# Optimization experiments

Measured on AMD Instinct MI355X. Metric: run time of the kernel, lower is better.

## Reference

```python
import jax, jax.numpy as jnp
import numpy as np

# Faithful JAX port of the approxmatch algorithm (Fan et al. / PyTorch-EMDLoss CUDA kernel):
# iterative soft bipartite matching with annealed temperature levels -4^j for j=8..-1, then 0,
# tracking remaining capacities ('saturation') of both point sets.

EPS = 1e-9

def _approx_match(xyz1, xyz2):
    # xyz1: [B,N,D], xyz2: [B,M,D] -> match: [B,N,M]
    B, n, _ = xyz1.shape
    m = xyz2.shape[1]
    factorl = max(n, m) // n  # capacity per point in set 1
    factorr = max(n, m) // m  # capacity per point in set 2
    # pairwise squared distances [B,N,M]
    d2 = jnp.sum((xyz1[:, :, None, :] - xyz2[:, None, :, :]) ** 2, axis=-1)
    # annealing levels: -4^8, -4^7, ..., -4^-1, 0
    levels = jnp.array([-(4.0 ** j) for j in range(8, -2, -1)] + [0.0],
                       dtype=xyz1.dtype)
    satl0 = jnp.full((B, n), float(factorl), dtype=xyz1.dtype)
    satr0 = jnp.full((B, m), float(factorr), dtype=xyz1.dtype)
    match0 = jnp.zeros((B, n, m), dtype=xyz1.dtype)

    def step(carry, level):
        satl, satr, match = carry
        # soft assignment weights scaled by remaining capacity of set 2
        w = jnp.exp(level * d2) * satr[:, None, :]                      # [B,N,M]
        # row-normalize, scaled by remaining capacity of set 1
        w = w / (jnp.sum(w, axis=2, keepdims=True) + EPS) * satl[:, :, None]
        # column capacity clipping
        ss = jnp.sum(w, axis=1) + EPS                                   # [B,M]
        r = jnp.minimum(satr / ss, 1.0)
        w = w * r[:, None, :]
        satr = jnp.maximum(satr - jnp.sum(w, axis=1), 0.0)
        satl = jnp.maximum(satl - jnp.sum(w, axis=2), 0.0)
        return (satl, satr, match + w), None

    (_, _, match), _ = jax.lax.scan(step, (satl0, satr0, match0), levels)
    return match


def setup_inputs() -> dict:
    key = jax.random.key(0)
    k1, k2 = jax.random.split(key)
    xyz1 = jax.random.normal(k1, (8, 2048, 3), dtype=jnp.float32)
    xyz2 = jax.random.normal(k2, (8, 2048, 3), dtype=jnp.float32)
    return {"xyz1": xyz1, "xyz2": xyz2}


def reference(xyz1, xyz2):
    # EMD cost per batch element: sum_{k,l} match[k,l] * ||x1_k - x2_l||
    match = _approx_match(xyz1, xyz2)                                   # [B,N,M]
    d = jnp.sqrt(jnp.sum((xyz1[:, :, None, :] - xyz2[:, None, :, :]) ** 2,
                         axis=-1))                                      # [B,N,M]
    return jnp.sum(match * d, axis=(1, 2))                              # [B]
```

## Files before the change

### kernel.cpp

```cpp
#include <hip/hip_runtime.h>
#include <math.h>

static constexpr int   B_   = 8;
static constexpr int   N_   = 2048;
static constexpr int   TPB  = 256;
static constexpr int   TILE = 32;
static constexpr int   NBLK = (B_ * N_) / TILE;
static constexpr int   BN   = B_ * N_;
static constexpr float EPS_ = 1e-9f;

#define WS_X1    (ws)
#define WS_X2    (ws + 4*BN)
#define WS_SATL  (ws + 8*BN)
#define WS_SATR  (ws + 9*BN)
#define WS_SCAL  (ws + 10*BN)
#define WS_LSCAL (ws + 11*BN)
#define WS_LSATR (ws + 12*BN)
#define WS_WR    (ws + 13*BN)
#define WS_LWR   (ws + 14*BN)
#define WS_COST  (ws + 15*BN)

__global__ void __launch_bounds__(TPB)
emd_init(const float* __restrict__ xyz1, const float* __restrict__ xyz2,
         float* __restrict__ ws)
{
    const int idx = blockIdx.x * TPB + threadIdx.x;
    if (idx >= BN) return;
    float x = xyz1[idx*3], y = xyz1[idx*3+1], z = xyz1[idx*3+2];
    reinterpret_cast<float4*>(WS_X1)[idx] =
        make_float4(x, y, z, fmaf(x,x, fmaf(y,y, z*z)));
    x = xyz2[idx*3]; y = xyz2[idx*3+1]; z = xyz2[idx*3+2];
    reinterpret_cast<float4*>(WS_X2)[idx] =
        make_float4(x, y, z, fmaf(x,x, fmaf(y,y, z*z)));
    WS_SATL[idx] = 1.f;
    WS_SATR[idx] = 1.f;
    WS_LSATR[idx] = 0.f;
    WS_COST[idx] = 0.f;
}

template<int MODE>
__global__ void __launch_bounds__(TPB)
emd_pass(float* __restrict__ ws, const float lvlA, const float lvlB)
{
    __shared__ float4 pts[N_];
    __shared__ float  auxA[N_];
    __shared__ float  auxB[N_];
    __shared__ float  red[64][33];

    const int b    = blockIdx.x >> 6;
    const int tile = blockIdx.x & 63;
    const int t    = threadIdx.x;
    const int g    = t & 3;
    const int c    = t >> 2;

    const float4* src = (MODE == 1)
        ? reinterpret_cast<const float4*>(WS_X1) + b * N_
        : reinterpret_cast<const float4*>(WS_X2) + b * N_;
    const float* aA = (MODE == 0) ? (WS_LSATR + b * N_)
                     : (MODE == 1) ? (WS_LSCAL + b * N_)
                     : (MODE == 2) ? (WS_LWR   + b * N_)
                                   : (WS_WR    + b * N_);
    const float* aB = WS_LSATR + b * N_;
    for (int p = t; p < N_; p += TPB) {
        pts[p]  = src[p];
        auxA[p] = aA[p];
        if (MODE == 2) auxB[p] = aB[p];
    }

    const float4* ownv = (MODE == 1)
        ? reinterpret_cast<const float4*>(WS_X2)
        : reinterpret_cast<const float4*>(WS_X1);
    const int obase = b * N_ + tile * TILE + g * 8;
    float cx[8], cy[8], cz[8], cq[8];
#pragma unroll
    for (int j = 0; j < 8; ++j) {
        float4 v = ownv[obase + j];
        cx[j] = -2.f * v.x; cy[j] = -2.f * v.y; cz[j] = -2.f * v.z;
        cq[j] = v.w;
    }
    __syncthreads();

    float s1[8], s2[8], s3[8];
#pragma unroll
    for (int j = 0; j < 8; ++j) { s1[j] = 0.f; s2[j] = 0.f; s3[j] = 0.f; }

    for (int i = 0; i < 32; ++i) {
        const int l = c + (i << 6);
        const float4 p = pts[l];
        const float  wA = auxA[l];
        float wB;
        if (MODE == 2) wB = auxB[l];
#pragma unroll
        for (int j = 0; j < 8; ++j) {
            const float s0 = p.w + cq[j];
            const float d2 = fmaf(cx[j], p.x,
                             fmaf(cy[j], p.y,
                             fmaf(cz[j], p.z, s0)));
            if (MODE == 0 || MODE == 1) {
                s1[j] += __builtin_amdgcn_exp2f(fmaf(lvlB, d2, wA));
            } else if (MODE == 2) {
                const float sq = __builtin_amdgcn_sqrtf(fmaxf(d2, 0.f));
                const float eA = __builtin_amdgcn_exp2f(fmaf(lvlA, d2, wA));
                s1[j] += eA;
                s2[j]  = fmaf(eA, sq, s2[j]);
                s3[j] += __builtin_amdgcn_exp2f(fmaf(lvlB, d2, wB));
            } else {
                const float sq = __builtin_amdgcn_sqrtf(fmaxf(d2, 0.f));
                s2[j] = fmaf(wA, sq, s2[j]);
            }
        }
    }

    float rs1 = 0.f, rs2 = 0.f, rs3 = 0.f;
    if (MODE != 3) {
#pragma unroll
        for (int j = 0; j < 8; ++j) red[c][g * 8 + j] = s1[j];
        __syncthreads();
        if (t < TILE) for (int cc = 0; cc < 64; ++cc) rs1 += red[cc][t];
    }
    if (MODE >= 2) {
        if (MODE != 3) __syncthreads();
#pragma unroll
        for (int j = 0; j < 8; ++j) red[c][g * 8 + j] = s2[j];
        __syncthreads();
        if (t < TILE) for (int cc = 0; cc < 64; ++cc) rs2 += red[cc][t];
    }
    if (MODE == 2) {
        __syncthreads();
#pragma unroll
        for (int j = 0; j < 8; ++j) red[c][g * 8 + j] = s3[j];
        __syncthreads();
        if (t < TILE) for (int cc = 0; cc < 64; ++cc) rs3 += red[cc][t];
    }

    if (t < TILE) {
        const int idx = b * N_ + tile * TILE + t;
        if (MODE == 0) {
            const float sc = WS_SATL[idx] / (rs1 + EPS_);
            WS_SCAL[idx]  = sc;
            WS_LSCAL[idx] = __log2f(sc);
        } else if (MODE == 1) {
            const float sr  = WS_SATR[idx];
            const float w1s = sr * rs1;
            const float rr  = fminf(sr / (w1s + EPS_), 1.f);
            const float wrv = sr * rr;
            const float srn = fmaxf(sr - rr * w1s, 0.f);
            WS_WR[idx]    = wrv;
            WS_LWR[idx]   = __log2f(wrv);
            WS_SATR[idx]  = srn;
            WS_LSATR[idx] = __log2f(srn);
        } else if (MODE == 2) {
            const float scp  = WS_SCAL[idx];
            const float sln  = fmaxf(WS_SATL[idx] - scp * rs1, 0.f);
            WS_COST[idx]     = fmaf(scp, rs2, WS_COST[idx]);
            const float scn  = sln / (rs3 + EPS_);
            WS_SATL[idx]  = sln;
            WS_SCAL[idx]  = scn;
            WS_LSCAL[idx] = __log2f(scn);
        } else {
            WS_COST[idx] = fmaf(WS_SCAL[idx], rs2, WS_COST[idx]);
        }
    }
}

__global__ void __launch_bounds__(TPB)
emd_finish(const float* __restrict__ cost, float* __restrict__ out)
{
    const int b = blockIdx.x;
    const int t = threadIdx.x;
    float v = 0.f;
    for (int i = t; i < N_; i += TPB) v += cost[b * N_ + i];
#pragma unroll
    for (int k = 32; k >= 1; k >>= 1) v += __shfl_xor(v, k, 64);
    __shared__ float wsum[4];
    if ((t & 63) == 0) wsum[t >> 6] = v;
    __syncthreads();
    if (t == 0) out[b] = wsum[0] + wsum[1] + wsum[2] + wsum[3];
}

extern "C" void kernel_launch(void* const* d_in, const int* in_sizes, int n_in,
                              void* d_out, int out_size, void* d_ws, size_t ws_size,
                              hipStream_t stream)
{
    const float* xyz1 = (const float*)d_in[0];
    const float* xyz2 = (const float*)d_in[1];
    float* out = (float*)d_out;
    float* ws  = (float*)d_ws;

    emd_init<<<BN / TPB, TPB, 0, stream>>>(xyz1, xyz2, ws);

    static const float levels[11] = {
        -65536.f, -16384.f, -4096.f, -1024.f, -256.f,
        -64.f, -16.f, -4.f, -1.f, -0.25f, 0.f};
    const float LOG2E = 1.4426950408889634f;

    emd_pass<0><<<NBLK, TPB, 0, stream>>>(ws, 0.f, levels[0] * LOG2E);
    emd_pass<1><<<NBLK, TPB, 0, stream>>>(ws, 0.f, levels[0] * LOG2E);
    for (int lev = 1; lev < 11; ++lev) {
        emd_pass<2><<<NBLK, TPB, 0, stream>>>(ws, levels[lev-1] * LOG2E,
                                                  levels[lev]   * LOG2E);
        emd_pass<1><<<NBLK, TPB, 0, stream>>>(ws, 0.f, levels[lev] * LOG2E);
    }
    emd_pass<3><<<NBLK, TPB, 0, stream>>>(ws, 0.f, 0.f);

    emd_finish<<<B_, TPB, 0, stream>>>(WS_COST, out);
}
```

Measured before the change: 352.3 us.

## Fuse all annealing passes into one persistent kernel with per-batch grid barriers

Replaces the 23 separate pass launches and the finish kernel with a single persistent kernel. Its 512 blocks sync per batch through atomic counter barriers, and per-point saturation, scale and cost stay in registers instead of round-tripping through global memory. The level factor is folded into the precomputed coefficients and shared-memory aux arrays, which saves a multiply per pair, and the block reduction becomes two-stage. The risks are deadlock if not all blocks are co-resident (it relies on 2 blocks per CU, with a spin timeout), plus barrier spin overhead.

```diff
diff --git a/kernel.cpp b/kernel.cpp
--- a/kernel.cpp
+++ b/kernel.cpp
@@ -5,47 +5,112 @@
 static constexpr int   N_   = 2048;
 static constexpr int   TPB  = 256;
 static constexpr int   TILE = 32;
-static constexpr int   NBLK = (B_ * N_) / TILE;
+static constexpr int   BPB  = 64;
+static constexpr int   NBLK = B_ * BPB;
 static constexpr int   BN   = B_ * N_;
 static constexpr float EPS_ = 1e-9f;
+static constexpr float LOG2E = 1.4426950408889634f;
 
 #define WS_X1    (ws)
 #define WS_X2    (ws + 4*BN)
-#define WS_SATL  (ws + 8*BN)
-#define WS_SATR  (ws + 9*BN)
-#define WS_SCAL  (ws + 10*BN)
-#define WS_LSCAL (ws + 11*BN)
-#define WS_LSATR (ws + 12*BN)
-#define WS_WR    (ws + 13*BN)
-#define WS_LWR   (ws + 14*BN)
-#define WS_COST  (ws + 15*BN)
+#define WS_LSCAL (ws + 8*BN)
+#define WS_LSATR (ws + 9*BN)
+#define WS_LWR   (ws + 10*BN)
+#define WS_WR    (ws + 11*BN)
+#define WS_COSTP (ws + 12*BN)
+#define WS_BARU  ((unsigned*)(ws + 12*BN + NBLK))
+
+__device__ __constant__ float c_lvl[11] = {
+    -65536.f*LOG2E, -16384.f*LOG2E, -4096.f*LOG2E, -1024.f*LOG2E,
+    -256.f*LOG2E,   -64.f*LOG2E,    -16.f*LOG2E,   -4.f*LOG2E,
+    -1.f*LOG2E,     -0.25f*LOG2E,   0.f };
 
 __global__ void __launch_bounds__(TPB)
 emd_init(const float* __restrict__ xyz1, const float* __restrict__ xyz2,
          float* __restrict__ ws)
 {
     const int idx = blockIdx.x * TPB + threadIdx.x;
-    if (idx >= BN) return;
-    float x = xyz1[idx*3], y = xyz1[idx*3+1], z = xyz1[idx*3+2];
-    reinterpret_cast<float4*>(WS_X1)[idx] =
-        make_float4(x, y, z, fmaf(x,x, fmaf(y,y, z*z)));
-    x = xyz2[idx*3]; y = xyz2[idx*3+1]; z = xyz2[idx*3+2];
-    reinterpret_cast<float4*>(WS_X2)[idx] =
-        make_float4(x, y, z, fmaf(x,x, fmaf(y,y, z*z)));
-    WS_SATL[idx] = 1.f;
-    WS_SATR[idx] = 1.f;
-    WS_LSATR[idx] = 0.f;
-    WS_COST[idx] = 0.f;
+    if (idx < BN) {
+        float x = xyz1[idx*3], y = xyz1[idx*3+1], z = xyz1[idx*3+2];
+        reinterpret_cast<float4*>(WS_X1)[idx] =
+            make_float4(x, y, z, fmaf(x,x, fmaf(y,y, z*z)));
+        x = xyz2[idx*3]; y = xyz2[idx*3+1]; z = xyz2[idx*3+2];
+        reinterpret_cast<float4*>(WS_X2)[idx] =
+            make_float4(x, y, z, fmaf(x,x, fmaf(y,y, z*z)));
+        WS_LSATR[idx] = 0.f;
+    }
+    if (idx < 8 * 64) WS_BARU[idx] = 0u;
+}
+
+__device__ __forceinline__ void bbar(unsigned* cnt, unsigned* gen, unsigned target)
+{
+    __syncthreads();
+    if (threadIdx.x == 0) {
+        __threadfence();
+        unsigned prev = __hip_atomic_fetch_add(cnt, 1u, __ATOMIC_ACQ_REL,
+                                               __HIP_MEMORY_SCOPE_AGENT);
+        if (prev == BPB - 1) {
+            __hip_atomic_store(cnt, 0u, __ATOMIC_RELAXED, __HIP_MEMORY_SCOPE_AGENT);
+            __hip_atomic_fetch_add(gen, 1u, __ATOMIC_ACQ_REL, __HIP_MEMORY_SCOPE_AGENT);
+        } else {
+            int spins = 0;
+            while (__hip_atomic_load(gen, __ATOMIC_ACQUIRE,
+                                     __HIP_MEMORY_SCOPE_AGENT) < target) {
+                __builtin_amdgcn_s_sleep(1);
+                if (++spins > (1 << 26)) break;
+            }
+        }
+        __threadfence();
+    }
+    __syncthreads();
 }
 
 template<int MODE>
-__global__ void __launch_bounds__(TPB)
-emd_pass(float* __restrict__ ws, const float lvlA, const float lvlB)
+__device__ __forceinline__ void sweep(
+    const float4* pts, const float* auxA, const float* auxB,
+    const float (&kx)[8], const float (&ky)[8], const float (&kz)[8],
+    const float (&kq)[8], float lvlA, float lvlB, int c,
+    float (&s1)[8], float (&s2)[8], float (&s3)[8])
+{
+    for (int i = 0; i < 32; ++i) {
+        const int l = c + (i << 6);
+        const float4 p = pts[l];
+        const float  wA = auxA[l];
+        float wB = 0.f;
+        if (MODE == 2) wB = auxB[l];
+#pragma unroll
+        for (int j = 0; j < 8; ++j) {
+            if (MODE == 0 || MODE == 1) {
+                const float arg = fmaf(kx[j], p.x, fmaf(ky[j], p.y,
+                                  fmaf(kz[j], p.z, wA + kq[j])));
+                s1[j] += __builtin_amdgcn_exp2f(arg);
+            } else if (MODE == 2) {
+                const float dotq = fmaf(kx[j], p.x, fmaf(ky[j], p.y,
+                                   fmaf(kz[j], p.z, kq[j])));
+                const float sq = __builtin_amdgcn_sqrtf(fmaxf(p.w + dotq, 0.f));
+                const float eA = __builtin_amdgcn_exp2f(fmaf(lvlA, dotq, wA));
+                const float eB = __builtin_amdgcn_exp2f(fmaf(lvlB, dotq, wB));
+                s1[j] += eA;
+                s2[j]  = fmaf(eA, sq, s2[j]);
+                s3[j] += eB;
+            } else {
+                const float dotq = fmaf(kx[j], p.x, fmaf(ky[j], p.y,
+                                   fmaf(kz[j], p.z, kq[j])));
+                const float sq = __builtin_amdgcn_sqrtf(fmaxf(p.w + dotq, 0.f));
+                s2[j] = fmaf(wA, sq, s2[j]);
+            }
+        }
+    }
+}
+
+__global__ void __launch_bounds__(TPB, 2)
+emd_main(float* __restrict__ ws, float* __restrict__ out)
 {
     __shared__ float4 pts[N_];
     __shared__ float  auxA[N_];
     __shared__ float  auxB[N_];
     __shared__ float  red[64][33];
+    __shared__ float  red2[8][33];
 
     const int b    = blockIdx.x >> 6;
     const int tile = blockIdx.x & 63;
@@ -53,129 +118,143 @@
     const int g    = t & 3;
     const int c    = t >> 2;
 
-    const float4* src = (MODE == 1)
-        ? reinterpret_cast<const float4*>(WS_X1) + b * N_
-        : reinterpret_cast<const float4*>(WS_X2) + b * N_;
-    const float* aA = (MODE == 0) ? (WS_LSATR + b * N_)
-                     : (MODE == 1) ? (WS_LSCAL + b * N_)
-                     : (MODE == 2) ? (WS_LWR   + b * N_)
-                                   : (WS_WR    + b * N_);
-    const float* aB = WS_LSATR + b * N_;
-    for (int p = t; p < N_; p += TPB) {
-        pts[p]  = src[p];
-        auxA[p] = aA[p];
-        if (MODE == 2) auxB[p] = aB[p];
-    }
-
-    const float4* ownv = (MODE == 1)
-        ? reinterpret_cast<const float4*>(WS_X2)
-        : reinterpret_cast<const float4*>(WS_X1);
-    const int obase = b * N_ + tile * TILE + g * 8;
-    float cx[8], cy[8], cz[8], cq[8];
-#pragma unroll
-    for (int j = 0; j < 8; ++j) {
-        float4 v = ownv[obase + j];
-        cx[j] = -2.f * v.x; cy[j] = -2.f * v.y; cz[j] = -2.f * v.z;
-        cq[j] = v.w;
-    }
-    __syncthreads();
-
+    unsigned* bcnt = WS_BARU + b * 64;
+    unsigned* bgen = bcnt + 32;
+    unsigned  mygen = 0;
+
+    const float4* x1v = reinterpret_cast<const float4*>(WS_X1) + b * N_;
+    const float4* x2v = reinterpret_cast<const float4*>(WS_X2) + b * N_;
+    const float* lscal = WS_LSCAL + b * N_;
+    const float* lsatr = WS_LSATR + b * N_;
+    const float* lwr   = WS_LWR   + b * N_;
+    const float* wrr   = WS_WR    + b * N_;
+
+    float rx[8], ry[8], rz[8], rq[8], ox[8], oy[8], oz[8], oq[8];
+    {
+        const int ob = tile * TILE + g * 8;
+#pragma unroll
+        for (int j = 0; j < 8; ++j) {
+            float4 v = x1v[ob + j];
+            rx[j] = -2.f*v.x; ry[j] = -2.f*v.y; rz[j] = -2.f*v.z; rq[j] = v.w;
+            float4 w = x2v[ob + j];
+            ox[j] = -2.f*w.x; oy[j] = -2.f*w.y; oz[j] = -2.f*w.z; oq[j] = w.w;
+        }
+    }
+
+    float satl = 1.f, satr = 1.f, mysc = 0.f, cost = 0.f;
+    const int gidx = b * N_ + tile * TILE + t;
     float s1[8], s2[8], s3[8];
-#pragma unroll
+    float kx[8], ky[8], kz[8], kq[8];
+
+#define ZERO3() _Pragma("unroll") \
     for (int j = 0; j < 8; ++j) { s1[j] = 0.f; s2[j] = 0.f; s3[j] = 0.f; }
 
-    for (int i = 0; i < 32; ++i) {
-        const int l = c + (i << 6);
-        const float4 p = pts[l];
-        const float  wA = auxA[l];
-        float wB;
-        if (MODE == 2) wB = auxB[l];
+#define REDUCE(arr, dst)                                                   \
+    {   _Pragma("unroll")                                                  \
+        for (int j = 0; j < 8; ++j) red[c][g * 8 + j] = arr[j];            \
+        __syncthreads();                                                   \
+        { const int o = t & 31, sg = t >> 5; float a = 0.f;                \
+          _Pragma("unroll")                                                \
+          for (int k = 0; k < 8; ++k) a += red[sg * 8 + k][o];             \
+          red2[sg][o] = a; }                                               \
+        __syncthreads();                                                   \
+        dst = 0.f;                                                         \
+        if (t < TILE) { _Pragma("unroll")                                  \
+            for (int sgg = 0; sgg < 8; ++sgg) dst += red2[sgg][t]; }       \
+        __syncthreads(); }
+
+    {
+        const float lv = c_lvl[0];
+        for (int p = t; p < N_; p += TPB) {
+            float4 v = x2v[p]; pts[p] = v;
+            auxA[p] = fmaf(lv, v.w, lsatr[p]);
+        }
 #pragma unroll
         for (int j = 0; j < 8; ++j) {
-            const float s0 = p.w + cq[j];
-            const float d2 = fmaf(cx[j], p.x,
-                             fmaf(cy[j], p.y,
-                             fmaf(cz[j], p.z, s0)));
-            if (MODE == 0 || MODE == 1) {
-                s1[j] += __builtin_amdgcn_exp2f(fmaf(lvlB, d2, wA));
-            } else if (MODE == 2) {
-                const float sq = __builtin_amdgcn_sqrtf(fmaxf(d2, 0.f));
-                const float eA = __builtin_amdgcn_exp2f(fmaf(lvlA, d2, wA));
-                s1[j] += eA;
-                s2[j]  = fmaf(eA, sq, s2[j]);
-                s3[j] += __builtin_amdgcn_exp2f(fmaf(lvlB, d2, wB));
-            } else {
-                const float sq = __builtin_amdgcn_sqrtf(fmaxf(d2, 0.f));
-                s2[j] = fmaf(wA, sq, s2[j]);
-            }
-        }
-    }
-
-    float rs1 = 0.f, rs2 = 0.f, rs3 = 0.f;
-    if (MODE != 3) {
-#pragma unroll
-        for (int j = 0; j < 8; ++j) red[c][g * 8 + j] = s1[j];
+            kx[j] = lv*rx[j]; ky[j] = lv*ry[j]; kz[j] = lv*rz[j]; kq[j] = lv*rq[j];
+        }
         __syncthreads();
-        if (t < TILE) for (int cc = 0; cc < 64; ++cc) rs1 += red[cc][t];
-    }
-    if (MODE >= 2) {
-        if (MODE != 3) __syncthreads();
-#pragma unroll
-        for (int j = 0; j < 8; ++j) red[c][g * 8 + j] = s2[j];
-        __syncthreads();
-        if (t < TILE) for (int cc = 0; cc < 64; ++cc) rs2 += red[cc][t];
-    }
-    if (MODE == 2) {
-        __syncthreads();
-#pragma unroll
-        for (int j = 0; j < 8; ++j) red[c][g * 8 + j] = s3[j];
-        __syncthreads();
-        if (t < TILE) for (int cc = 0; cc < 64; ++cc) rs3 += red[cc][t];
-    }
-
-    if (t < TILE) {
-        const int idx = b * N_ + tile * TILE + t;
-        if (MODE == 0) {
-            const float sc = WS_SATL[idx] / (rs1 + EPS_);
-            WS_SCAL[idx]  = sc;
-            WS_LSCAL[idx] = __log2f(sc);
-        } else if (MODE == 1) {
-            const float sr  = WS_SATR[idx];
-            const float w1s = sr * rs1;
-            const float rr  = fminf(sr / (w1s + EPS_), 1.f);
-            const float wrv = sr * rr;
-            const float srn = fmaxf(sr - rr * w1s, 0.f);
-            WS_WR[idx]    = wrv;
-            WS_LWR[idx]   = __log2f(wrv);
-            WS_SATR[idx]  = srn;
-            WS_LSATR[idx] = __log2f(srn);
-        } else if (MODE == 2) {
-            const float scp  = WS_SCAL[idx];
-            const float sln  = fmaxf(WS_SATL[idx] - scp * rs1, 0.f);
-            WS_COST[idx]     = fmaf(scp, rs2, WS_COST[idx]);
-            const float scn  = sln / (rs3 + EPS_);
-            WS_SATL[idx]  = sln;
-            WS_SCAL[idx]  = scn;
-            WS_LSCAL[idx] = __log2f(scn);
+        ZERO3();
+        sweep<0>(pts, auxA, auxB, kx, ky, kz, kq, 0.f, 0.f, c, s1, s2, s3);
+        float rs1; REDUCE(s1, rs1);
+        if (t < TILE) {
+            mysc = satl / (rs1 + EPS_);
+            WS_LSCAL[gidx] = __log2f(mysc);
+        }
+        bbar(bcnt, bgen, ++mygen);
+    }
+
+    for (int lev = 0; lev <= 10; ++lev) {
+        {
+            const float lv = c_lvl[lev];
+            for (int p = t; p < N_; p += TPB) {
+                float4 v = x1v[p]; pts[p] = v;
+                auxA[p] = fmaf(lv, v.w, lscal[p]);
+            }
+#pragma unroll
+            for (int j = 0; j < 8; ++j) {
+                kx[j] = lv*ox[j]; ky[j] = lv*oy[j]; kz[j] = lv*oz[j]; kq[j] = lv*oq[j];
+            }
+            __syncthreads();
+            ZERO3();
+            sweep<1>(pts, auxA, auxB, kx, ky, kz, kq, 0.f, 0.f, c, s1, s2, s3);
+            float rs1; REDUCE(s1, rs1);
+            if (t < TILE) {
+                const float w1s = satr * rs1;
+                const float rr  = fminf(satr / (w1s + EPS_), 1.f);
+                const float wrv = satr * rr;
+                satr = fmaxf(satr - rr * w1s, 0.f);
+                WS_WR[gidx]    = wrv;
+                WS_LWR[gidx]   = __log2f(wrv);
+                WS_LSATR[gidx] = __log2f(satr);
+            }
+            bbar(bcnt, bgen, ++mygen);
+        }
+
+        if (lev < 10) {
+            const float lvA = c_lvl[lev], lvB = c_lvl[lev + 1];
+            for (int p = t; p < N_; p += TPB) {
+                float4 v = x2v[p]; pts[p] = v;
+                auxA[p] = fmaf(lvA, v.w, lwr[p]);
+                auxB[p] = fmaf(lvB, v.w, lsatr[p]);
+            }
+            __syncthreads();
+            ZERO3();
+            sweep<2>(pts, auxA, auxB, rx, ry, rz, rq, lvA, lvB, c, s1, s2, s3);
+            float rs1, rs2, rs3;
+            REDUCE(s1, rs1); REDUCE(s2, rs2); REDUCE(s3, rs3);
+            if (t < TILE) {
+                satl = fmaxf(satl - mysc * rs1, 0.f);
+                cost = fmaf(mysc, rs2, cost);
+                mysc = satl / (rs3 + EPS_);
+                WS_LSCAL[gidx] = __log2f(mysc);
+            }
+            bbar(bcnt, bgen, ++mygen);
         } else {
-            WS_COST[idx] = fmaf(WS_SCAL[idx], rs2, WS_COST[idx]);
-        }
-    }
-}
-
-__global__ void __launch_bounds__(TPB)
-emd_finish(const float* __restrict__ cost, float* __restrict__ out)
-{
-    const int b = blockIdx.x;
-    const int t = threadIdx.x;
-    float v = 0.f;
-    for (int i = t; i < N_; i += TPB) v += cost[b * N_ + i];
-#pragma unroll
-    for (int k = 32; k >= 1; k >>= 1) v += __shfl_xor(v, k, 64);
-    __shared__ float wsum[4];
-    if ((t & 63) == 0) wsum[t >> 6] = v;
-    __syncthreads();
-    if (t == 0) out[b] = wsum[0] + wsum[1] + wsum[2] + wsum[3];
+            for (int p = t; p < N_; p += TPB) {
+                float4 v = x2v[p]; pts[p] = v;
+                auxA[p] = wrr[p];
+            }
+            __syncthreads();
+            ZERO3();
+            sweep<3>(pts, auxA, auxB, rx, ry, rz, rq, 0.f, 0.f, c, s1, s2, s3);
+            float rs2; REDUCE(s2, rs2);
+            if (t < TILE) {
+                cost = fmaf(mysc, rs2, cost);
+                float v = cost;
+#pragma unroll
+                for (int k = 16; k >= 1; k >>= 1) v += __shfl_xor(v, k, 64);
+                if (t == 0) WS_COSTP[b * BPB + tile] = v;
+            }
+            bbar(bcnt, bgen, ++mygen);
+            if (tile == 0 && t < 64) {
+                float v = WS_COSTP[b * BPB + t];
+#pragma unroll
+                for (int k = 32; k >= 1; k >>= 1) v += __shfl_xor(v, k, 64);
+                if (t == 0) out[b] = v;
+            }
+        }
+    }
 }
 
 extern "C" void kernel_launch(void* const* d_in, const int* in_sizes, int n_in,
@@ -188,20 +267,5 @@
     float* ws  = (float*)d_ws;
 
     emd_init<<<BN / TPB, TPB, 0, stream>>>(xyz1, xyz2, ws);
-
-    static const float levels[11] = {
-        -65536.f, -16384.f, -4096.f, -1024.f, -256.f,
-        -64.f, -16.f, -4.f, -1.f, -0.25f, 0.f};
-    const float LOG2E = 1.4426950408889634f;
-
-    emd_pass<0><<<NBLK, TPB, 0, stream>>>(ws, 0.f, levels[0] * LOG2E);
-    emd_pass<1><<<NBLK, TPB, 0, stream>>>(ws, 0.f, levels[0] * LOG2E);
-    for (int lev = 1; lev < 11; ++lev) {
-        emd_pass<2><<<NBLK, TPB, 0, stream>>>(ws, levels[lev-1] * LOG2E,
-                                                  levels[lev]   * LOG2E);
-        emd_pass<1><<<NBLK, TPB, 0, stream>>>(ws, 0.f, levels[lev] * LOG2E);
-    }
-    emd_pass<3><<<NBLK, TPB, 0, stream>>>(ws, 0.f, 0.f);
-
-    emd_finish<<<B_, TPB, 0, stream>>>(WS_COST, out);
-}
+    emd_main<<<NBLK, TPB, 0, stream>>>(ws, out);
+}
```

Result: slower. 993.2 us (+181.9%).
